# Kernel tuning notes

Measured on AMD Instinct MI355X. Metric: run time of the kernel, lower is better.

## Reference

```python
import jax, jax.numpy as jnp
import numpy as np


def setup_inputs() -> dict:
    key = jax.random.key(0)
    k1, k2, k3, k4 = jax.random.split(key, 4)
    B, C = 32768, 10
    x = jax.random.normal(k1, (B, 1, 28, 28), dtype=jnp.float32)
    linear_weight = jax.random.normal(k2, (4 * 14 * 14 + 1 + 2, C), dtype=jnp.float32)
    linear_bias = jax.random.normal(k3, (C,), dtype=jnp.float32)
    sampler_weights = jax.random.normal(k4, (4,), dtype=jnp.float32)
    return {"x": x, "linear_weight": linear_weight, "linear_bias": linear_bias,
            "sampler_weights": sampler_weights}


def reference(x, linear_weight, linear_bias, sampler_weights):
    # Closed-form simulation of the 4-qubit circuits:
    # RY(t)|0> -> <Z>=cos(t); after CX(0,1): <Z1> = cos(t0)*cos(t1); CX(2,3) likewise.
    B = x.shape[0]
    # Extract non-overlapping 2x2 patches in row-major order -> (B, 196, 4)
    p = x[:, 0].reshape(B, 14, 2, 14, 2).transpose(0, 1, 3, 2, 4).reshape(B, 196, 4)
    c = jnp.cos(p)
    # quanvolution_circuit per patch: [cos a, cos a cos b, cos c, cos c cos d]
    feats = jnp.stack([c[..., 0], c[..., 0] * c[..., 1],
                       c[..., 2], c[..., 2] * c[..., 3]], axis=-1)  # (B,196,4)
    qfeat = feats.reshape(B, 784)
    # fully_connected_circuit on qfeat[:, :4]: mean of the four post-CX <Z>
    cf = jnp.cos(qfeat[:, :4])
    qfc = (cf[:, 0] + cf[:, 0] * cf[:, 1] + cf[:, 2] + cf[:, 2] * cf[:, 3]) / 4.0  # (B,)
    # sampler_circuit: sequential RY angles add on wires 0 and 1
    t0 = qfeat[:, 0] + sampler_weights[0] + sampler_weights[2]
    t1 = qfeat[:, 1] + sampler_weights[1] + sampler_weights[3]
    z0 = jnp.cos(t0)
    z1 = z0 * jnp.cos(t1)
    sampler = jax.nn.softmax(jnp.stack([z0, z1], axis=-1), axis=-1)  # (B,2)
    combined = jnp.concatenate([qfeat, qfc[:, None], sampler], axis=-1)  # (B,787)
    logits = combined @ linear_weight + linear_bias
    return jax.nn.log_softmax(logits, axis=-1)
```

## Files before the change

### kernel.cpp

```cpp
#include <hip/hip_runtime.h>


typedef __attribute__((ext_vector_type(8))) short short8;
typedef __attribute__((ext_vector_type(4))) float floatx4;

__device__ __forceinline__ unsigned short f2bf(float f) {
    unsigned u = __float_as_uint(f);
    return (unsigned short)((u + 0x7FFFu + ((u >> 16) & 1u)) >> 16);
}

#define A_OFF  28672
#define QF_OFF 61440

__global__ __launch_bounds__(256, 2)
void qml_mfma(const float* __restrict__ x,
              const float* __restrict__ wm,
              const float* __restrict__ bias,
              const float* __restrict__ sw,
              float* __restrict__ out,
              int B)
{
    __shared__ __align__(16) char smem[62464];
    float* rawW = (float*)(smem + A_OFF);
    float* qf   = (float*)(smem + QF_OFF);
    float* lg   = (float*)(smem + A_OFF);

    const int t = threadIdx.x;
    const int lane = t & 63;
    const int wv = __builtin_amdgcn_readfirstlane((int)(t >> 6));
    const int g = blockIdx.x;

    for (int i = t; i < 7870; i += 256) rawW[i] = wm[i];
    __syncthreads();

#pragma unroll
    for (int c = 0; c < 7; ++c) {
        const int CH = c * 256 + t;
        const int T = CH >> 6, L = CH & 63;
        const int n = L & 15, kq = L >> 4;
        short8 v;
#pragma unroll
        for (int j = 0; j < 8; ++j) {
            const int kh = 32 * T + kq * 8 + j;
            const int sg = kh >> 7, kl = kh & 127;
            float w = 0.0f;
            if (kl < 112 && n < 10) w = rawW[(112 * sg + kl) * 10 + n];
            v[j] = (short)f2bf(w);
        }
        *(short8*)(smem + CH * 16) = v;
    }
    __syncthreads();

    int st_pr[4], st_s[4], st_unit[4];
    const float* st_px[4];
#pragma unroll
    for (int c4 = 0; c4 < 4; ++c4) {
        const int G = c4 * 256 + t;
        const int s = G >> 4, pr = G & 15;
        st_s[c4] = s; st_pr[c4] = pr;
        st_unit[c4] = s * 16 + (pr ^ (s & 15));
        int sglob = g * 64 + s; if (sglob >= B) sglob = B - 1;
        const int r = (pr >= 7) ? 1 : 0;
        const int cq = (pr >= 7) ? (pr - 7) : pr;
        st_px[c4] = x + (size_t)sglob * 784 + r * 56 + 4 * cq;
    }

    floatx4 tp[4], bt[4];

    const int sA = wv * 16 + (lane & 15);
    const int swzA = sA & 15;
    const int prq = lane >> 4;

    floatx4 acc = {0.f, 0.f, 0.f, 0.f};

#pragma unroll
    for (int c4 = 0; c4 < 4; ++c4)
        if (st_pr[c4] < 14) {
            tp[c4] = *(const floatx4*)(st_px[c4]);
            bt[c4] = *(const floatx4*)(st_px[c4] + 28);
        }
#pragma unroll
    for (int c4 = 0; c4 < 4; ++c4) {
        float f0 = 0.f, f1 = 0.f, f2 = 0.f, f3 = 0.f;
        float f4 = 0.f, f5 = 0.f, f6 = 0.f, f7 = 0.f;
        if (st_pr[c4] < 14) {
            const float c0 = __cosf(tp[c4].x), c1 = __cosf(tp[c4].y);
            const float c2 = __cosf(bt[c4].x), c3 = __cosf(bt[c4].y);
            f0 = c0; f1 = c0 * c1; f2 = c2; f3 = c2 * c3;
            const float c4_ = __cosf(tp[c4].z), c5 = __cosf(tp[c4].w);
            const float c6 = __cosf(bt[c4].z), c7 = __cosf(bt[c4].w);
            f4 = c4_; f5 = c4_ * c5; f6 = c6; f7 = c6 * c7;
            if (st_pr[c4] == 0) {
                float* qd = qf + st_s[c4] * 4;
                qd[0] = f0; qd[1] = f1; qd[2] = f2; qd[3] = f3;
            }
        }
        short8 v;
        v[0] = (short)f2bf(f0); v[1] = (short)f2bf(f1);
        v[2] = (short)f2bf(f2); v[3] = (short)f2bf(f3);
        v[4] = (short)f2bf(f4); v[5] = (short)f2bf(f5);
        v[6] = (short)f2bf(f6); v[7] = (short)f2bf(f7);
        *(short8*)(smem + A_OFF + st_unit[c4] * 16) = v;
    }
    __syncthreads();

#pragma unroll
    for (int sg = 0; sg < 7; ++sg) {
        const int buf = sg & 1;

        if (sg < 6) {
#pragma unroll
            for (int c4 = 0; c4 < 4; ++c4)
                if (st_pr[c4] < 14) {
                    tp[c4] = *(const floatx4*)(st_px[c4] + (sg + 1) * 112);
                    bt[c4] = *(const floatx4*)(st_px[c4] + (sg + 1) * 112 + 28);
                }
        }

#pragma unroll
        for (int tl = 0; tl < 4; ++tl) {
            const int pr = 4 * tl + prq;
            const short8 a = *(const short8*)(smem + A_OFF + buf * 16384
                                              + (sA * 16 + (pr ^ swzA)) * 16);
            const short8 b = *(const short8*)(smem + ((4 * sg + tl) * 64 + lane) * 16);
            acc = __builtin_amdgcn_mfma_f32_16x16x32_bf16(a, b, acc, 0, 0, 0);
        }

        if (sg < 6) {
#pragma unroll
            for (int c4 = 0; c4 < 4; ++c4) {
                float f0 = 0.f, f1 = 0.f, f2 = 0.f, f3 = 0.f;
                float f4 = 0.f, f5 = 0.f, f6 = 0.f, f7 = 0.f;
                if (st_pr[c4] < 14) {
                    const float c0 = __cosf(tp[c4].x), c1 = __cosf(tp[c4].y);
                    const float c2 = __cosf(bt[c4].x), c3 = __cosf(bt[c4].y);
                    f0 = c0; f1 = c0 * c1; f2 = c2; f3 = c2 * c3;
                    const float c4_ = __cosf(tp[c4].z), c5 = __cosf(tp[c4].w);
                    const float c6 = __cosf(bt[c4].z), c7 = __cosf(bt[c4].w);
                    f4 = c4_; f5 = c4_ * c5; f6 = c6; f7 = c6 * c7;
                }
                short8 v;
                v[0] = (short)f2bf(f0); v[1] = (short)f2bf(f1);
                v[2] = (short)f2bf(f2); v[3] = (short)f2bf(f3);
                v[4] = (short)f2bf(f4); v[5] = (short)f2bf(f5);
                v[6] = (short)f2bf(f6); v[7] = (short)f2bf(f7);
                *(short8*)(smem + A_OFF + (buf ^ 1) * 16384 + st_unit[c4] * 16) = v;
            }
        }
        __syncthreads();
    }

    {
        const int n = lane & 15;
        const int rbase = wv * 16 + (lane >> 4) * 4;
        if (n < 10) {
#pragma unroll
            for (int r = 0; r < 4; ++r) lg[(rbase + r) * 11 + n] = acc[r];
        }
    }
    __syncthreads();

#pragma unroll
    for (int e = t; e < 640; e += 256) {
        const int s2 = e / 10, c2 = e - 10 * s2;
        float logit = lg[s2 * 11 + c2];
        const float q0 = qf[s2 * 4 + 0], q1 = qf[s2 * 4 + 1];
        const float q2 = qf[s2 * 4 + 2], q3 = qf[s2 * 4 + 3];

        const float f0 = __cosf(q0), f1 = __cosf(q1);
        const float f2 = __cosf(q2), f3 = __cosf(q3);
        const float qfc = (f0 + f0 * f1 + f2 + f2 * f3) * 0.25f;

        const float t0 = q0 + sw[0] + sw[2];
        const float t1 = q1 + sw[1] + sw[3];
        const float z0 = __cosf(t0);
        const float z1 = z0 * __cosf(t1);
        const float e0 = __expf(z0), e1 = __expf(z1);
        const float inv = 1.0f / (e0 + e1);

        const float* __restrict__ wt = wm + 7840;
        logit += bias[c2] + qfc * wt[c2] + (e0 * inv) * wt[10 + c2]
                          + (e1 * inv) * wt[20 + c2];
        lg[s2 * 11 + c2] = logit;
    }
    __syncthreads();

#pragma unroll
    for (int e = t; e < 640; e += 256) {
        const int s2 = e / 10, c2 = e - 10 * s2;
        float m = -3.4e38f;
#pragma unroll
        for (int k = 0; k < 10; ++k) m = fmaxf(m, lg[s2 * 11 + k]);
        float ss = 0.0f;
#pragma unroll
        for (int k = 0; k < 10; ++k) ss += __expf(lg[s2 * 11 + k] - m);
        const float lse = __logf(ss) + m;
        if (g * 64 + s2 < B)
            out[(size_t)g * 640 + e] = lg[s2 * 11 + c2] - lse;
    }
}

extern "C" void kernel_launch(void* const* d_in, const int* in_sizes, int n_in,
                              void* d_out, int out_size, void* d_ws, size_t ws_size,
                              hipStream_t stream) {
    const float* x    = (const float*)d_in[0];
    const float* w    = (const float*)d_in[1];
    const float* bias = (const float*)d_in[2];
    const float* sw   = (const float*)d_in[3];
    float* out = (float*)d_out;

    const int B = in_sizes[0] / 784;
    const int nblk = (B + 63) / 64;
    qml_mfma<<<nblk, 256, 0, stream>>>(x, w, bias, sw, out, B);
}
```

Before: 162.2 us.

## Build MFMA A-operand in registers and triple-buffer global strip loads

```diff
diff --git a/kernel.cpp b/kernel.cpp
--- a/kernel.cpp
+++ b/kernel.cpp
@@ -9,8 +9,8 @@
     return (unsigned short)((u + 0x7FFFu + ((u >> 16) & 1u)) >> 16);
 }
 
-#define A_OFF  28672
-#define QF_OFF 61440
+#define SCR_OFF 28672
+#define QF_OFF  60160
 
 __global__ __launch_bounds__(256, 2)
 void qml_mfma(const float* __restrict__ x,
@@ -20,10 +20,10 @@
               float* __restrict__ out,
               int B)
 {
-    __shared__ __align__(16) char smem[62464];
-    float* rawW = (float*)(smem + A_OFF);
+    __shared__ __align__(16) char smem[61184];
+    float* rawW = (float*)(smem + SCR_OFF);
+    float* lg   = (float*)(smem + SCR_OFF);
     float* qf   = (float*)(smem + QF_OFF);
-    float* lg   = (float*)(smem + A_OFF);
 
     const int t = threadIdx.x;
     const int lane = t & 63;
@@ -51,103 +51,75 @@
     }
     __syncthreads();
 
-    int st_pr[4], st_s[4], st_unit[4];
-    const float* st_px[4];
+    const int m = lane & 15;
+    const int q = lane >> 4;
+    int sample = g * 64 + wv * 16 + m;
+    const bool s_ok = (sample < B);
+    if (sample >= B) sample = B - 1;
+    const float* __restrict__ xs = x + (size_t)sample * 784;
+
+    int offT[4], validT[4];
 #pragma unroll
-    for (int c4 = 0; c4 < 4; ++c4) {
-        const int G = c4 * 256 + t;
-        const int s = G >> 4, pr = G & 15;
-        st_s[c4] = s; st_pr[c4] = pr;
-        st_unit[c4] = s * 16 + (pr ^ (s & 15));
-        int sglob = g * 64 + s; if (sglob >= B) sglob = B - 1;
+    for (int T = 0; T < 4; ++T) {
+        const int pr = 4 * T + q;
+        validT[T] = (pr < 14);
         const int r = (pr >= 7) ? 1 : 0;
         const int cq = (pr >= 7) ? (pr - 7) : pr;
-        st_px[c4] = x + (size_t)sglob * 784 + r * 56 + 4 * cq;
+        offT[T] = validT[T] ? (r * 56 + 4 * cq) : 0;
     }
 
-    floatx4 tp[4], bt[4];
+    floatx4 tp[3][4], bt[3][4];
 
-    const int sA = wv * 16 + (lane & 15);
-    const int swzA = sA & 15;
-    const int prq = lane >> 4;
+#define LOADSTRIP(slot, sg_)                                            \
+    {                                                                   \
+        _Pragma("unroll")                                               \
+        for (int T = 0; T < 4; ++T) {                                   \
+            tp[slot][T] = *(const floatx4*)(xs + (sg_) * 112 + offT[T]);        \
+            bt[slot][T] = *(const floatx4*)(xs + (sg_) * 112 + offT[T] + 28);   \
+        }                                                               \
+    }
 
     floatx4 acc = {0.f, 0.f, 0.f, 0.f};
 
-#pragma unroll
-    for (int c4 = 0; c4 < 4; ++c4)
-        if (st_pr[c4] < 14) {
-            tp[c4] = *(const floatx4*)(st_px[c4]);
-            bt[c4] = *(const floatx4*)(st_px[c4] + 28);
-        }
-#pragma unroll
-    for (int c4 = 0; c4 < 4; ++c4) {
-        float f0 = 0.f, f1 = 0.f, f2 = 0.f, f3 = 0.f;
-        float f4 = 0.f, f5 = 0.f, f6 = 0.f, f7 = 0.f;
-        if (st_pr[c4] < 14) {
-            const float c0 = __cosf(tp[c4].x), c1 = __cosf(tp[c4].y);
-            const float c2 = __cosf(bt[c4].x), c3 = __cosf(bt[c4].y);
-            f0 = c0; f1 = c0 * c1; f2 = c2; f3 = c2 * c3;
-            const float c4_ = __cosf(tp[c4].z), c5 = __cosf(tp[c4].w);
-            const float c6 = __cosf(bt[c4].z), c7 = __cosf(bt[c4].w);
-            f4 = c4_; f5 = c4_ * c5; f6 = c6; f7 = c6 * c7;
-            if (st_pr[c4] == 0) {
-                float* qd = qf + st_s[c4] * 4;
-                qd[0] = f0; qd[1] = f1; qd[2] = f2; qd[3] = f3;
-            }
-        }
-        short8 v;
-        v[0] = (short)f2bf(f0); v[1] = (short)f2bf(f1);
-        v[2] = (short)f2bf(f2); v[3] = (short)f2bf(f3);
-        v[4] = (short)f2bf(f4); v[5] = (short)f2bf(f5);
-        v[6] = (short)f2bf(f6); v[7] = (short)f2bf(f7);
-        *(short8*)(smem + A_OFF + st_unit[c4] * 16) = v;
-    }
-    __syncthreads();
+    LOADSTRIP(0, 0)
+    LOADSTRIP(1, 1)
 
 #pragma unroll
     for (int sg = 0; sg < 7; ++sg) {
-        const int buf = sg & 1;
-
-        if (sg < 6) {
-#pragma unroll
-            for (int c4 = 0; c4 < 4; ++c4)
-                if (st_pr[c4] < 14) {
-                    tp[c4] = *(const floatx4*)(st_px[c4] + (sg + 1) * 112);
-                    bt[c4] = *(const floatx4*)(st_px[c4] + (sg + 1) * 112 + 28);
-                }
+        const int slot = sg % 3;
+        if (sg < 5) {
+            const int ns = (sg + 2) % 3;
+            LOADSTRIP(ns, sg + 2)
         }
 
 #pragma unroll
-        for (int tl = 0; tl < 4; ++tl) {
-            const int pr = 4 * tl + prq;
-            const short8 a = *(const short8*)(smem + A_OFF + buf * 16384
-                                              + (sA * 16 + (pr ^ swzA)) * 16);
-            const short8 b = *(const short8*)(smem + ((4 * sg + tl) * 64 + lane) * 16);
-            acc = __builtin_amdgcn_mfma_f32_16x16x32_bf16(a, b, acc, 0, 0, 0);
+        for (int T = 0; T < 4; ++T) {
+            const floatx4 P = tp[slot][T];
+            const floatx4 Q = bt[slot][T];
+            const float c0 = __cosf(P.x), c1 = __cosf(P.y);
+            const float c2 = __cosf(Q.x), c3 = __cosf(Q.y);
+            const float c4 = __cosf(P.z), c5 = __cosf(P.w);
+            const float c6 = __cosf(Q.z), c7 = __cosf(Q.w);
+            const float f0 = c0, f1 = c0 * c1, f2 = c2, f3 = c2 * c3;
+            const float f4 = c4, f5 = c4 * c5, f6 = c6, f7 = c6 * c7;
+
+            if (sg == 0 && T == 0 && q == 0) {
+                float* qd = qf + (wv * 16 + m) * 4;
+                qd[0] = f0; qd[1] = f1; qd[2] = f2; qd[3] = f3;
+            }
+
+            short8 a;
+            a[0] = (short)f2bf(f0); a[1] = (short)f2bf(f1);
+            a[2] = (short)f2bf(f2); a[3] = (short)f2bf(f3);
+            a[4] = (short)f2bf(f4); a[5] = (short)f2bf(f5);
+            a[6] = (short)f2bf(f6); a[7] = (short)f2bf(f7);
+            if (!validT[T]) {
+                a = (short8){0, 0, 0, 0, 0, 0, 0, 0};
+            }
+
+            const short8 b8 = *(const short8*)(smem + ((4 * sg + T) * 64 + lane) * 16);
+            acc = __builtin_amdgcn_mfma_f32_16x16x32_bf16(a, b8, acc, 0, 0, 0);
         }
-
-        if (sg < 6) {
-#pragma unroll
-            for (int c4 = 0; c4 < 4; ++c4) {
-                float f0 = 0.f, f1 = 0.f, f2 = 0.f, f3 = 0.f;
-                float f4 = 0.f, f5 = 0.f, f6 = 0.f, f7 = 0.f;
-                if (st_pr[c4] < 14) {
-                    const float c0 = __cosf(tp[c4].x), c1 = __cosf(tp[c4].y);
-                    const float c2 = __cosf(bt[c4].x), c3 = __cosf(bt[c4].y);
-                    f0 = c0; f1 = c0 * c1; f2 = c2; f3 = c2 * c3;
-                    const float c4_ = __cosf(tp[c4].z), c5 = __cosf(tp[c4].w);
-                    const float c6 = __cosf(bt[c4].z), c7 = __cosf(bt[c4].w);
-                    f4 = c4_; f5 = c4_ * c5; f6 = c6; f7 = c6 * c7;
-                }
-                short8 v;
-                v[0] = (short)f2bf(f0); v[1] = (short)f2bf(f1);
-                v[2] = (short)f2bf(f2); v[3] = (short)f2bf(f3);
-                v[4] = (short)f2bf(f4); v[5] = (short)f2bf(f5);
-                v[6] = (short)f2bf(f6); v[7] = (short)f2bf(f7);
-                *(short8*)(smem + A_OFF + (buf ^ 1) * 16384 + st_unit[c4] * 16) = v;
-            }
-        }
-        __syncthreads();
     }
 
     {
@@ -188,13 +160,13 @@
 #pragma unroll
     for (int e = t; e < 640; e += 256) {
         const int s2 = e / 10, c2 = e - 10 * s2;
-        float m = -3.4e38f;
+        float mx = -3.4e38f;
 #pragma unroll
-        for (int k = 0; k < 10; ++k) m = fmaxf(m, lg[s2 * 11 + k]);
+        for (int k = 0; k < 10; ++k) mx = fmaxf(mx, lg[s2 * 11 + k]);
         float ss = 0.0f;
 #pragma unroll
-        for (int k = 0; k < 10; ++k) ss += __expf(lg[s2 * 11 + k] - m);
-        const float lse = __logf(ss) + m;
+        for (int k = 0; k < 10; ++k) ss += __expf(lg[s2 * 11 + k] - mx);
+        const float lse = __logf(ss) + mx;
         if (g * 64 + s2 < B)
             out[(size_t)g * 640 + e] = lg[s2 * 11 + c2] - lse;
     }
```

Measured after the change: 161.3 us. No clear change (-0.6%).
